# Performance work log

Hardware: AMD Instinct MI355X
Metric: run time of the kernel (lower is better)

## Reference

```python
import jax, jax.numpy as jnp
import numpy as np

B, D, S, NSYM, V, T = 4096, 128, 16, 128, 128, 8
EPS = 1e-6; ACT_TH = 0.9999; GBS = 0.8; CC = 0.01
sg = jax.lax.stop_gradient


def clin(xr, xi, Wr, Wi):
    # ComplexLinear: torch Linear applies x @ W.T
    return xr @ Wr.T - xi @ Wi.T, xi @ Wr.T + xr @ Wi.T


def cnorm(zr, zi, scale, shift):
    # ComplexLayerNorm: normalize magnitude (torch .var is unbiased -> ddof=1), keep phase
    mag = jnp.sqrt(zr * zr + zi * zi) + EPS
    mean = mag.mean(-1, keepdims=True)
    var = jnp.var(mag, axis=-1, ddof=1, keepdims=True)
    nm = (mag - mean) / jnp.sqrt(var + EPS) * scale + shift
    ph = jnp.arctan2(zi, zr)
    return nm * jnp.cos(ph), nm * jnp.sin(ph)


def modrelu(zr, zi, bias):
    norm = jnp.sqrt(zr * zr + zi * zi) + EPS
    s = jax.nn.relu(norm + bias) / norm
    return zr * s, zi * s


def setup_inputs():
    key = jax.random.key(0)
    ks = jax.random.split(key, 18)
    n = lambda k, sh, s=0.05: jax.random.normal(k, sh, jnp.float32) * s
    return dict(
        input_ids=jax.random.randint(ks[0], (B, 1), 0, V),
        emb_mag=n(ks[1], (V, D), 1.0),
        emb_phase=n(ks[2], (V, D), 1.0),
        cell_Wr=n(ks[3], (D, D), 0.08), cell_Wi=n(ks[4], (D, D), 0.08),
        ln_scale=jnp.ones((D,), jnp.float32), ln_shift=jnp.zeros((D,), jnp.float32),
        mod_bias=jnp.zeros((D,), jnp.float32),
        Wh=n(ks[5], (1, 2 * D)), bh=jnp.full((1,), -2.0, jnp.float32),
        Ws=n(ks[6], (3, 2 * D)), bs=jnp.zeros((3,), jnp.float32),
        Wq_r=n(ks[7], (D, D), 0.08), Wq_i=n(ks[8], (D, D), 0.08),
        Wk_r=n(ks[9], (D, D), 0.08), Wk_i=n(ks[10], (D, D), 0.08),
        Wv_r=n(ks[11], (D, D), 0.08), Wv_i=n(ks[12], (D, D), 0.08),
        codebook=jax.random.uniform(ks[13], (NSYM, 2 * D), jnp.float32, -0.5, 0.5),
        adjacency=n(ks[14], (NSYM, NSYM), 0.1),
        Wd=n(ks[15], (V, 2 * D)), bd=jnp.zeros((V,), jnp.float32),
    )


def _forward(input_ids, emb_mag, emb_phase, cell_Wr, cell_Wi, ln_scale, ln_shift,
             mod_bias, Wh, bh, Ws, bs, Wq_r, Wq_i, Wk_r, Wk_i, Wv_r, Wv_i,
             codebook, adjacency, Wd, bd):
    idx = input_ids[:, 0]                              # (B,)
    r = emb_mag[idx]; th = emb_phase[idx]
    zr, zi = r * jnp.cos(th), r * jnp.sin(th)          # complex embed (B,D)
    bsz = zr.shape[0]
    stack_mem = jnp.zeros((bsz, S, 2 * D), jnp.float32)
    ptr = jnp.zeros((bsz, S), jnp.float32).at[:, 0].set(1.0)
    halting = jnp.zeros((bsz, 1), jnp.float32)
    remain = jnp.ones((bsz, 1), jnp.float32)
    zwr = jnp.zeros_like(zr); zwi = jnp.zeros_like(zi)
    vq_total = jnp.zeros((bsz,), jnp.float32)
    eth_total = jnp.zeros((bsz,), jnp.float32)
    ponder = jnp.zeros((bsz, 1), jnp.float32)
    cur_sym = None
    scale = D ** -0.5
    for t in range(T):  # fixed small recursion depth, unrolled
        # AdaptiveRecursiveCell
        pr, pi = clin(zr, zi, cell_Wr, cell_Wi)
        pr, pi = cnorm(pr, pi, ln_scale, ln_shift)
        pr, pi = modrelu(pr, pi, mod_bias)
        qr, qi = clin(pr, pi, Wq_r, Wq_i)
        kr, ki = clin(pr, pi, Wk_r, Wk_i)
        vr, vi = clin(pr, pi, Wv_r, Wv_i)
        qf = jnp.concatenate([qr, qi], -1)
        kf = jnp.concatenate([kr, ki], -1)
        attn = jax.nn.softmax(qf @ kf.T * scale, axis=-1)  # (B,B) cross-batch attn, as in source
        ar, ai2 = attn @ vr, attn @ vi
        zf = jnp.concatenate([ar, ai2], -1)                # (B,2D)
        p_halt = jax.nn.sigmoid(zf @ Wh.T + bh)            # (B,1)
        ctrl = jax.nn.softmax(zf @ Ws.T + bs, axis=-1)     # (B,3)
        # DifferentiableStack soft push/pop
        push, pop, noop = ctrl[:, 0:1], ctrl[:, 1:2], ctrl[:, 2:3]
        ptr_up = jnp.roll(ptr, 1, axis=1)
        ptr_dn = jnp.roll(ptr, -1, axis=1)
        new_ptr = push * ptr_up + pop * ptr_dn + noop * ptr
        new_ptr = new_ptr / (new_ptr.sum(1, keepdims=True) + EPS)
        wm = (push * ptr_up)[:, :, None]                   # (B,S,1) soft write mask
        stack_mem = wm * zf[:, None, :] + stack_mem * (1.0 - wm)
        read = (stack_mem * new_ptr[:, :, None]).sum(1)    # (B,2D)
        ptr = new_ptr
        cr, ci = ar + read[:, :D], ai2 + read[:, D:]
        # GraphMemoryVQ
        cf = jnp.concatenate([cr, ci], -1)
        d = (cf * cf).sum(-1, keepdims=True) + (codebook * codebook).sum(-1) - 2.0 * cf @ codebook.T
        if cur_sym is not None:
            d = d - GBS * jax.nn.sigmoid(adjacency[cur_sym])
        sym = jnp.argmin(d, axis=-1)
        zq = codebook[sym]
        vq_loss = ((zq - sg(cf)) ** 2).mean(-1) + CC * ((sg(zq) - cf) ** 2).mean(-1)
        zq_st = cf + sg(zq - cf)                            # straight-through
        # EthicalConstraint: CE(adjacency[prev], curr)
        if cur_sym is None:
            eth = jnp.zeros((bsz,), jnp.float32)
        else:
            logp = jax.nn.log_softmax(adjacency[cur_sym], axis=-1)
            eth = -jnp.take_along_axis(logp, sym[:, None], axis=-1)[:, 0]
        eth_total = eth_total + eth
        cur_sym = sym
        zr = 0.7 * cr + 0.3 * zq_st[:, :D]
        zi = 0.7 * ci + 0.3 * zq_st[:, D:]
        # ACT halting (standard ACT weighting; final step takes remainder)
        still = (halting < ACT_TH).astype(jnp.float32)
        p = p_halt * still
        if t == T - 1:
            p = remain
        halting = halting + p
        remain = remain - p
        zwr = zwr + p * zr
        zwi = zwi + p * zi
        vq_total = vq_total + vq_loss
        ponder = ponder + still
    logits = jnp.concatenate([zwr, zwi], -1) @ Wd.T + bd    # (B, V)
    return logits, vq_total, eth_total, ponder[:, 0]


def reference(input_ids, emb_mag, emb_phase, cell_Wr, cell_Wi, ln_scale, ln_shift,
              mod_bias, Wh, bh, Ws, bs, Wq_r, Wq_i, Wk_r, Wk_i, Wv_r, Wv_i,
              codebook, adjacency, Wd, bd):
    return _forward(input_ids, emb_mag, emb_phase, cell_Wr, cell_Wi, ln_scale, ln_shift,
                    mod_bias, Wh, bh, Ws, bs, Wq_r, Wq_i, Wk_r, Wk_i, Wv_r, Wv_i,
                    codebook, adjacency, Wd, bd)
```

## Files before the change

kernel.cpp:

```cpp
#include <hip/hip_runtime.h>
#include <hip/hip_bf16.h>
#include <math.h>

#define B 4096
#define D 128
#define TWO_D 256
#define S_SLOTS 16
#define NSYM 128
#define V_OUT 128
#define T_STEPS 8
#define EPS 1e-6f
#define ACT_TH 0.9999f
#define GBS 0.8f
#define CC 0.01f
#define SCALE 0.08838834764831845f

#define NCHUNK 8
#define CHUNK (B / NCHUNK)
#define QT 32
#define KT 64

typedef short s16x8 __attribute__((ext_vector_type(8)));
typedef float f32x4 __attribute__((ext_vector_type(4)));
#define MFMA16(A, Bb, C) __builtin_amdgcn_mfma_f32_16x16x32_bf16(A, Bb, C, 0, 0, 0)

__device__ __forceinline__ unsigned short f2bf(float x) {
  __bf16 h = (__bf16)x;
  return *(unsigned short*)&h;
}
__device__ __forceinline__ float bf2f(unsigned short u) {
  __bf16 h = *(__bf16*)&u;
  return (float)h;
}

__device__ __forceinline__ float combine_w(const float* __restrict__ Wr,
                                           const float* __restrict__ Wi,
                                           int j, int k) {
  if (j < D) return (k < D) ? Wr[j * D + k] : -Wi[j * D + (k - D)];
  return (k < D) ? Wi[(j - D) * D + k] : Wr[(j - D) * D + (k - D)];
}

__global__ __launch_bounds__(256) void build_weights(
    const float* __restrict__ cell_Wr, const float* __restrict__ cell_Wi,
    const float* __restrict__ Wq_r, const float* __restrict__ Wq_i,
    const float* __restrict__ Wk_r, const float* __restrict__ Wk_i,
    const float* __restrict__ Wv_r, const float* __restrict__ Wv_i,
    const float* __restrict__ codebook,
    unsigned short* __restrict__ cellWH, unsigned short* __restrict__ cellWL,
    unsigned short* __restrict__ qkvWH, unsigned short* __restrict__ qkvWL,
    float* __restrict__ cbsq) {
  int e = blockIdx.x * 256 + threadIdx.x;
  int j = e >> 8, k = e & 255;
  float v = combine_w(cell_Wr, cell_Wi, j, k);
  unsigned short hh = f2bf(v);
  cellWH[e] = hh; cellWL[e] = f2bf(v - bf2f(hh));
  v = combine_w(Wq_r, Wq_i, j, k);
  hh = f2bf(v); qkvWH[e] = hh; qkvWL[e] = f2bf(v - bf2f(hh));
  v = combine_w(Wk_r, Wk_i, j, k);
  hh = f2bf(v); qkvWH[65536 + e] = hh; qkvWL[65536 + e] = f2bf(v - bf2f(hh));
  v = combine_w(Wv_r, Wv_i, j, k);
  hh = f2bf(v); qkvWH[131072 + e] = hh; qkvWL[131072 + e] = f2bf(v - bf2f(hh));
  if (blockIdx.x == 0 && threadIdx.x < NSYM) {
    float s = 0.f;
    for (int c = 0; c < TWO_D; c++) {
      float cv = codebook[threadIdx.x * TWO_D + c];
      s += cv * cv;
    }
    cbsq[threadIdx.x] = s;
  }
}

__global__ __launch_bounds__(128) void init_state(
    const int* __restrict__ input_ids, const float* __restrict__ emb_mag,
    const float* __restrict__ emb_phase,
    unsigned short* __restrict__ zfH, unsigned short* __restrict__ zfL,
    float* __restrict__ ptrb, float* __restrict__ halting,
    float* __restrict__ remain, float* __restrict__ vq,
    float* __restrict__ eth, float* __restrict__ ponder,
    float* __restrict__ zw, float* __restrict__ stack) {
  int b = blockIdx.x, tid = threadIdx.x;
  int idx = input_ids[b];
  float rr = emb_mag[idx * D + tid];
  float th = emb_phase[idx * D + tid];
  float zr = rr * cosf(th), zi = rr * sinf(th);
  unsigned short hh = f2bf(zr);
  zfH[(size_t)b * TWO_D + tid] = hh;
  zfL[(size_t)b * TWO_D + tid] = f2bf(zr - bf2f(hh));
  hh = f2bf(zi);
  zfH[(size_t)b * TWO_D + D + tid] = hh;
  zfL[(size_t)b * TWO_D + D + tid] = f2bf(zi - bf2f(hh));
  zw[(size_t)b * TWO_D + tid] = 0.f;
  zw[(size_t)b * TWO_D + D + tid] = 0.f;
  if (tid < S_SLOTS) ptrb[b * S_SLOTS + tid] = (tid == 0) ? 1.f : 0.f;
  if (tid == 0) {
    halting[b] = 0.f; remain[b] = 1.f;
    vq[b] = 0.f; eth[b] = 0.f; ponder[b] = 0.f;
  }
  for (int k = tid; k < S_SLOTS * TWO_D; k += 128)
    stack[(size_t)b * S_SLOTS * TWO_D + k] = 0.f;
}

template <int MODE>
__global__ __launch_bounds__(256) void gemm_mfma(
    const unsigned short* __restrict__ AH, const unsigned short* __restrict__ AL,
    const unsigned short* __restrict__ WH, const unsigned short* __restrict__ WL,
    float* __restrict__ Cf,
    unsigned short* __restrict__ qH_, unsigned short* __restrict__ qL_,
    unsigned short* __restrict__ kH_, unsigned short* __restrict__ kL_,
    unsigned short* __restrict__ vtH_, unsigned short* __restrict__ vtL_) {
  const int tid = threadIdx.x;
  const int w = tid >> 6, lane = tid & 63, r = lane & 15, h = lane >> 4;
  const int m0 = blockIdx.x * 32 + (w & 1) * 16;
  const int n0g = blockIdx.y * 64 + (w >> 1) * 32;
  f32x4 acc[2];
  acc[0] = f32x4{0.f, 0.f, 0.f, 0.f};
  acc[1] = f32x4{0.f, 0.f, 0.f, 0.f};
  const size_t abase = (size_t)(m0 + r) * TWO_D;
  const size_t wb0 = (size_t)(n0g + r) * TWO_D;
  const size_t wb1 = (size_t)(n0g + 16 + r) * TWO_D;
#pragma unroll
  for (int kf = 0; kf < 8; kf++) {
    s16x8 ah = *(const s16x8*)&AH[abase + kf * 32 + h * 8];
    s16x8 al = *(const s16x8*)&AL[abase + kf * 32 + h * 8];
    s16x8 b0h = *(const s16x8*)&WH[wb0 + kf * 32 + h * 8];
    s16x8 b0l = *(const s16x8*)&WL[wb0 + kf * 32 + h * 8];
    s16x8 b1h = *(const s16x8*)&WH[wb1 + kf * 32 + h * 8];
    s16x8 b1l = *(const s16x8*)&WL[wb1 + kf * 32 + h * 8];
    acc[0] = MFMA16(ah, b0h, acc[0]);
    acc[0] = MFMA16(ah, b0l, acc[0]);
    acc[0] = MFMA16(al, b0h, acc[0]);
    acc[1] = MFMA16(ah, b1h, acc[1]);
    acc[1] = MFMA16(ah, b1l, acc[1]);
    acc[1] = MFMA16(al, b1h, acc[1]);
  }
#pragma unroll
  for (int ct = 0; ct < 2; ct++) {
    int col = n0g + ct * 16 + r;
#pragma unroll
    for (int reg = 0; reg < 4; reg++) {
      int row = m0 + h * 4 + reg;
      float val = acc[ct][reg];
      if (MODE == 0) {
        Cf[(size_t)row * TWO_D + col] = val;
      } else {
        int buf = col >> 8;
        int c = col & 255;
        if (buf == 0) {
          float v2 = val * SCALE;
          unsigned short hh = f2bf(v2);
          qH_[(size_t)row * TWO_D + c] = hh;
          qL_[(size_t)row * TWO_D + c] = f2bf(v2 - bf2f(hh));
        } else if (buf == 1) {
          unsigned short hh = f2bf(val);
          kH_[(size_t)row * TWO_D + c] = hh;
          kL_[(size_t)row * TWO_D + c] = f2bf(val - bf2f(hh));
        } else {
          unsigned short hh = f2bf(val);
          vtH_[(size_t)c * B + row] = hh;
          vtL_[(size_t)c * B + row] = f2bf(val - bf2f(hh));
        }
      }
    }
  }
}

__global__ __launch_bounds__(128) void cnorm_modrelu(
    const float* __restrict__ pf, const float* __restrict__ ln_scale,
    const float* __restrict__ ln_shift, const float* __restrict__ mod_bias,
    unsigned short* __restrict__ pfH, unsigned short* __restrict__ pfL) {
  int b = blockIdx.x, d = threadIdx.x;
  __shared__ float red[128];
  float pr = pf[(size_t)b * TWO_D + d];
  float pi = pf[(size_t)b * TWO_D + D + d];
  float h = sqrtf(pr * pr + pi * pi);
  float mag = h + EPS;
  red[d] = mag;
  __syncthreads();
  for (int s = 64; s > 0; s >>= 1) {
    if (d < s) red[d] += red[d + s];
    __syncthreads();
  }
  float mean = red[0] * (1.f / 128.f);
  __syncthreads();
  float dm = mag - mean;
  red[d] = dm * dm;
  __syncthreads();
  for (int s = 64; s > 0; s >>= 1) {
    if (d < s) red[d] += red[d + s];
    __syncthreads();
  }
  float var = red[0] * (1.f / 127.f);
  float nm = dm * (1.f / sqrtf(var + EPS)) * ln_scale[d] + ln_shift[d];
  float cph, sph;
  if (h > 0.f) { cph = pr / h; sph = pi / h; } else { cph = 1.f; sph = 0.f; }
  float zr = nm * cph, zi = nm * sph;
  float norm = sqrtf(zr * zr + zi * zi) + EPS;
  float s = fmaxf(norm + mod_bias[d], 0.f) / norm;
  float or_ = zr * s, oi_ = zi * s;
  unsigned short hh = f2bf(or_);
  pfH[(size_t)b * TWO_D + d] = hh;
  pfL[(size_t)b * TWO_D + d] = f2bf(or_ - bf2f(hh));
  hh = f2bf(oi_);
  pfH[(size_t)b * TWO_D + D + d] = hh;
  pfL[(size_t)b * TWO_D + D + d] = f2bf(oi_ - bf2f(hh));
}

__global__ __launch_bounds__(256) void flash_mfma(
    const unsigned short* __restrict__ qH, const unsigned short* __restrict__ qL,
    const unsigned short* __restrict__ kH, const unsigned short* __restrict__ kL,
    const unsigned short* __restrict__ vtH, const unsigned short* __restrict__ vtL,
    float* __restrict__ Opart, float* __restrict__ mpart,
    float* __restrict__ lpart) {
  __shared__ float m_lds[QT], corr_lds[QT];
  __shared__ float wmax[QT][2], lpart_lds[QT][2];
  __shared__ unsigned short Ph[QT][72], Pl[QT][72];
  const int tid = threadIdx.x;
  const int w = tid >> 6, lane = tid & 63;
  const int r = lane & 15, h = lane >> 4;
  const int qt = w & 1, kh = w >> 1;
  const int bid = blockIdx.x;
  const int chunk = bid & 7;
  const int q0 = (bid >> 3) * QT;

  s16x8 qfh[8], qfl[8];
  {
    const size_t base = (size_t)(q0 + qt * 16 + r) * TWO_D;
#pragma unroll
    for (int kf = 0; kf < 8; kf++) {
      qfh[kf] = *(const s16x8*)&qH[base + kf * 32 + h * 8];
      qfl[kf] = *(const s16x8*)&qL[base + kf * 32 + h * 8];
    }
  }
  f32x4 o[2][4];
#pragma unroll
  for (int qi = 0; qi < 2; qi++)
#pragma unroll
    for (int dt = 0; dt < 4; dt++) o[qi][dt] = f32x4{0.f, 0.f, 0.f, 0.f};
  float l_loc[4] = {0.f, 0.f, 0.f, 0.f};
  if (tid < QT) m_lds[tid] = -1e30f;
  __syncthreads();

  for (int kt = 0; kt < CHUNK / KT; kt++) {
    const int j0 = chunk * CHUNK + kt * KT;
    f32x4 sacc[2];
    sacc[0] = f32x4{0.f, 0.f, 0.f, 0.f};
    sacc[1] = f32x4{0.f, 0.f, 0.f, 0.f};
    const size_t kb0 = (size_t)(j0 + kh * 32 + r) * TWO_D;
    const size_t kb1 = (size_t)(j0 + kh * 32 + 16 + r) * TWO_D;
#pragma unroll
    for (int kf = 0; kf < 8; kf++) {
      s16x8 b0h = *(const s16x8*)&kH[kb0 + kf * 32 + h * 8];
      s16x8 b0l = *(const s16x8*)&kL[kb0 + kf * 32 + h * 8];
      s16x8 b1h = *(const s16x8*)&kH[kb1 + kf * 32 + h * 8];
      s16x8 b1l = *(const s16x8*)&kL[kb1 + kf * 32 + h * 8];
      sacc[0] = MFMA16(qfh[kf], b0h, sacc[0]);
      sacc[0] = MFMA16(qfh[kf], b0l, sacc[0]);
      sacc[0] = MFMA16(qfl[kf], b0h, sacc[0]);
      sacc[1] = MFMA16(qfh[kf], b1h, sacc[1]);
      sacc[1] = MFMA16(qfh[kf], b1l, sacc[1]);
      sacc[1] = MFMA16(qfl[kf], b1h, sacc[1]);
    }
#pragma unroll
    for (int reg = 0; reg < 4; reg++) {
      float v = fmaxf(sacc[0][reg], sacc[1][reg]);
      v = fmaxf(v, __shfl_xor(v, 1));
      v = fmaxf(v, __shfl_xor(v, 2));
      v = fmaxf(v, __shfl_xor(v, 4));
      v = fmaxf(v, __shfl_xor(v, 8));
      if (r == 0) wmax[qt * 16 + h * 4 + reg][kh] = v;
    }
    __syncthreads();
    if (lane < 8) {
      int row = w * 8 + lane;
      float mo = m_lds[row];
      float mn = fmaxf(mo, fmaxf(wmax[row][0], wmax[row][1]));
      corr_lds[row] = __expf(mo - mn);
      m_lds[row] = mn;
    }
    __syncthreads();
#pragma unroll
    for (int reg = 0; reg < 4; reg++) {
      int row = qt * 16 + h * 4 + reg;
      float mrow = m_lds[row];
      float p0 = __expf(sacc[0][reg] - mrow);
      float p1 = __expf(sacc[1][reg] - mrow);
      float rs = p0 + p1;
      rs += __shfl_xor(rs, 1);
      rs += __shfl_xor(rs, 2);
      rs += __shfl_xor(rs, 4);
      rs += __shfl_xor(rs, 8);
      l_loc[reg] = l_loc[reg] * corr_lds[row] + rs;
      unsigned short p0h = f2bf(p0), p1h = f2bf(p1);
      Ph[row][kh * 32 + r] = p0h;
      Pl[row][kh * 32 + r] = f2bf(p0 - bf2f(p0h));
      Ph[row][kh * 32 + 16 + r] = p1h;
      Pl[row][kh * 32 + 16 + r] = f2bf(p1 - bf2f(p1h));
    }
#pragma unroll
    for (int qi = 0; qi < 2; qi++)
#pragma unroll
      for (int reg = 0; reg < 4; reg++) {
        float c = corr_lds[qi * 16 + h * 4 + reg];
#pragma unroll
        for (int dt = 0; dt < 4; dt++) o[qi][dt][reg] *= c;
      }
    __syncthreads();
#pragma unroll
    for (int kf2 = 0; kf2 < 2; kf2++) {
      s16x8 pa_h[2], pa_l[2];
#pragma unroll
      for (int qi = 0; qi < 2; qi++) {
        pa_h[qi] = *(const s16x8*)&Ph[qi * 16 + r][kf2 * 32 + h * 8];
        pa_l[qi] = *(const s16x8*)&Pl[qi * 16 + r][kf2 * 32 + h * 8];
      }
#pragma unroll
      for (int dt = 0; dt < 4; dt++) {
        const size_t vb = (size_t)(w * 64 + dt * 16 + r) * B + j0 + kf2 * 32 + h * 8;
        s16x8 vh = *(const s16x8*)&vtH[vb];
        s16x8 vl = *(const s16x8*)&vtL[vb];
#pragma unroll
        for (int qi = 0; qi < 2; qi++) {
          o[qi][dt] = MFMA16(pa_h[qi], vh, o[qi][dt]);
          o[qi][dt] = MFMA16(pa_h[qi], vl, o[qi][dt]);
          o[qi][dt] = MFMA16(pa_l[qi], vh, o[qi][dt]);
        }
      }
    }
  }
  if (r == 0) {
#pragma unroll
    for (int reg = 0; reg < 4; reg++)
      lpart_lds[qt * 16 + h * 4 + reg][kh] = l_loc[reg];
  }
  __syncthreads();
  const size_t obase = (size_t)chunk * B + q0;
#pragma unroll
  for (int qi = 0; qi < 2; qi++)
#pragma unroll
    for (int reg = 0; reg < 4; reg++) {
      float* dst = &Opart[(obase + qi * 16 + h * 4 + reg) * TWO_D + w * 64 + r];
#pragma unroll
      for (int dt = 0; dt < 4; dt++) dst[dt * 16] = o[qi][dt][reg];
    }
  if (w == 0 && lane < QT) {
    mpart[chunk * B + q0 + lane] = m_lds[lane];
    lpart[chunk * B + q0 + lane] = lpart_lds[lane][0] + lpart_lds[lane][1];
  }
}

__global__ __launch_bounds__(256) void merge_attn(
    const float* __restrict__ Opart, const float* __restrict__ mpart,
    const float* __restrict__ lpart, float* __restrict__ af) {
  int b = blockIdx.x, c = threadIdx.x;
  float M = -1e30f;
#pragma unroll
  for (int ch = 0; ch < NCHUNK; ch++) M = fmaxf(M, mpart[ch * B + b]);
  float l = 0.f, o = 0.f;
#pragma unroll
  for (int ch = 0; ch < NCHUNK; ch++) {
    float wgt = __expf(mpart[ch * B + b] - M);
    l += lpart[ch * B + b] * wgt;
    o += Opart[((size_t)ch * B + b) * TWO_D + c] * wgt;
  }
  af[(size_t)b * TWO_D + c] = o / l;
}

__global__ __launch_bounds__(256) void step_kernel(
    const float* __restrict__ af, unsigned short* __restrict__ zfH,
    unsigned short* __restrict__ zfL, float* __restrict__ stack,
    float* __restrict__ ptrb, float* __restrict__ halting,
    float* __restrict__ remain, float* __restrict__ vq,
    float* __restrict__ eth, float* __restrict__ ponder,
    float* __restrict__ zw, int* __restrict__ cursym,
    const float* __restrict__ Wh, const float* __restrict__ bh,
    const float* __restrict__ Ws3, const float* __restrict__ bs3,
    const float* __restrict__ codebook, const float* __restrict__ cbsq,
    const float* __restrict__ adjacency, int t) {
  const int b = blockIdx.x, tid = threadIdx.x;
  __shared__ float cf_sh[TWO_D];
  __shared__ float r0[256], r1[256], r2[256], r3[256];
  __shared__ float nptr_sh[S_SLOTS], wm_sh[S_SLOTS];
  __shared__ float dist_sh[NSYM];
  __shared__ int idx_sh[NSYM];
  __shared__ float sc_sh[8];

  const float z_c = af[(size_t)b * TWO_D + tid];
  const int cs_old = (t > 0) ? cursym[b] : 0;

  r0[tid] = z_c * Wh[tid];
  r1[tid] = z_c * Ws3[tid];
  r2[tid] = z_c * Ws3[TWO_D + tid];
  r3[tid] = z_c * Ws3[2 * TWO_D + tid];
  __syncthreads();
  for (int s = 128; s > 0; s >>= 1) {
    if (tid < s) {
      r0[tid] += r0[tid + s]; r1[tid] += r1[tid + s];
      r2[tid] += r2[tid + s]; r3[tid] += r3[tid + s];
    }
    __syncthreads();
  }
  if (tid == 0) {
    float ph = 1.f / (1.f + expf(-(r0[0] + bh[0])));
    float l0 = r1[0] + bs3[0], l1 = r2[0] + bs3[1], l2 = r3[0] + bs3[2];
    float mx = fmaxf(l0, fmaxf(l1, l2));
    float e0 = expf(l0 - mx), e1 = expf(l1 - mx), e2 = expf(l2 - mx);
    float inv = 1.f / (e0 + e1 + e2);
    sc_sh[0] = e0 * inv; sc_sh[1] = e1 * inv; sc_sh[2] = e2 * inv;
    sc_sh[3] = ph;
  }
  __syncthreads();
  float push = sc_sh[0], pop = sc_sh[1], noop = sc_sh[2], p_halt = sc_sh[3];
  if (tid < S_SLOTS) {
    float pc = ptrb[b * S_SLOTS + tid];
    float pu = ptrb[b * S_SLOTS + ((tid + 15) & 15)];
    float pd = ptrb[b * S_SLOTS + ((tid + 1) & 15)];
    float raw = push * pu + pop * pd + noop * pc;
    float wmv = push * pu;
    float ssum = raw;
    for (int off = 1; off < 16; off <<= 1) ssum += __shfl_xor(ssum, off);
    float np_ = raw / (ssum + EPS);
    nptr_sh[tid] = np_;
    wm_sh[tid] = wmv;
    ptrb[b * S_SLOTS + tid] = np_;
  }
  __syncthreads();
  float acc = 0.f;
#pragma unroll
  for (int s = 0; s < S_SLOTS; s++) {
    size_t ix = ((size_t)(b * S_SLOTS + s)) * TWO_D + tid;
    float v = stack[ix];
    float wv = wm_sh[s];
    v = wv * z_c + v * (1.f - wv);
    stack[ix] = v;
    acc += v * nptr_sh[s];
  }
  float cf_c = z_c + acc;
  cf_sh[tid] = cf_c;
  r0[tid] = cf_c * cf_c;
  __syncthreads();
  for (int s = 128; s > 0; s >>= 1) {
    if (tid < s) r0[tid] += r0[tid + s];
    __syncthreads();
  }
  float cfsq = r0[0];
  if (tid < NSYM) {
    const float* cb = codebook + (size_t)tid * TWO_D;
    float dot = 0.f;
#pragma unroll 8
    for (int c = 0; c < TWO_D; c++) dot += cf_sh[c] * cb[c];
    float dval = cfsq + cbsq[tid] - 2.f * dot;
    if (t > 0) {
      float a = adjacency[cs_old * NSYM + tid];
      dval -= GBS * (1.f / (1.f + expf(-a)));
    }
    dist_sh[tid] = dval;
    idx_sh[tid] = tid;
  }
  __syncthreads();
  for (int s = 64; s > 0; s >>= 1) {
    if (tid < s) {
      float dA = dist_sh[tid], dB = dist_sh[tid + s];
      int iA = idx_sh[tid], iB = idx_sh[tid + s];
      if (dB < dA || (dB == dA && iB < iA)) {
        dist_sh[tid] = dB; idx_sh[tid] = iB;
      }
    }
    __syncthreads();
  }
  const int sym = idx_sh[0];
  const float zq_c = codebook[(size_t)sym * TWO_D + tid];
  float diff = zq_c - cf_c;
  r1[tid] = diff * diff;
  r2[tid] = (t > 0 && tid < NSYM) ? adjacency[cs_old * NSYM + tid] : -1e30f;
  __syncthreads();
  for (int s = 128; s > 0; s >>= 1) {
    if (tid < s) {
      r1[tid] += r1[tid + s];
      r2[tid] = fmaxf(r2[tid], r2[tid + s]);
    }
    __syncthreads();
  }
  float amax = r2[0];
  r3[tid] = (t > 0 && tid < NSYM) ? expf(adjacency[cs_old * NSYM + tid] - amax)
                                  : 0.f;
  __syncthreads();
  for (int s = 128; s > 0; s >>= 1) {
    if (tid < s) r3[tid] += r3[tid + s];
    __syncthreads();
  }
  if (tid == 0) {
    float vql = (1.f + CC) * (r1[0] * (1.f / (float)TWO_D));
    float h = halting[b], rem = remain[b];
    float still = (h < ACT_TH) ? 1.f : 0.f;
    float p = (t == T_STEPS - 1) ? rem : p_halt * still;
    halting[b] = h + p;
    remain[b] = rem - p;
    ponder[b] += still;
    vq[b] += vql;
    if (t > 0) {
      float asym = adjacency[cs_old * NSYM + sym];
      eth[b] += (amax + logf(r3[0]) - asym);
    }
    cursym[b] = sym;
    sc_sh[4] = p;
  }
  __syncthreads();
  float p = sc_sh[4];
  float znew = 0.7f * cf_c + 0.3f * zq_c;
  unsigned short hh = f2bf(znew);
  zfH[(size_t)b * TWO_D + tid] = hh;
  zfL[(size_t)b * TWO_D + tid] = f2bf(znew - bf2f(hh));
  zw[(size_t)b * TWO_D + tid] += p * znew;
}

__global__ __launch_bounds__(128) void logits_kernel(
    const float* __restrict__ zw, const float* __restrict__ Wd,
    const float* __restrict__ bd, const float* __restrict__ vq,
    const float* __restrict__ eth, const float* __restrict__ ponder,
    float* __restrict__ out) {
  int b = blockIdx.x, tid = threadIdx.x;
  __shared__ float zsh[TWO_D];
  zsh[tid] = zw[(size_t)b * TWO_D + tid];
  zsh[tid + D] = zw[(size_t)b * TWO_D + D + tid];
  __syncthreads();
  const float* wrow = Wd + (size_t)tid * TWO_D;
  float dot = 0.f;
#pragma unroll 8
  for (int c = 0; c < TWO_D; c++) dot += zsh[c] * wrow[c];
  out[(size_t)b * V_OUT + tid] = dot + bd[tid];
  if (tid == 0) {
    out[(size_t)B * V_OUT + b] = vq[b];
    out[(size_t)B * V_OUT + B + b] = eth[b];
    out[(size_t)B * V_OUT + 2 * B + b] = ponder[b];
  }
}

extern "C" void kernel_launch(void* const* d_in, const int* in_sizes, int n_in,
                              void* d_out, int out_size, void* d_ws,
                              size_t ws_size, hipStream_t stream) {
  const int* input_ids = (const int*)d_in[0];
  const float* emb_mag = (const float*)d_in[1];
  const float* emb_phase = (const float*)d_in[2];
  const float* cell_Wr = (const float*)d_in[3];
  const float* cell_Wi = (const float*)d_in[4];
  const float* ln_scale = (const float*)d_in[5];
  const float* ln_shift = (const float*)d_in[6];
  const float* mod_bias = (const float*)d_in[7];
  const float* Wh = (const float*)d_in[8];
  const float* bh = (const float*)d_in[9];
  const float* Ws3 = (const float*)d_in[10];
  const float* bs3 = (const float*)d_in[11];
  const float* Wq_r = (const float*)d_in[12];
  const float* Wq_i = (const float*)d_in[13];
  const float* Wk_r = (const float*)d_in[14];
  const float* Wk_i = (const float*)d_in[15];
  const float* Wv_r = (const float*)d_in[16];
  const float* Wv_i = (const float*)d_in[17];
  const float* codebook = (const float*)d_in[18];
  const float* adjacency = (const float*)d_in[19];
  const float* Wd = (const float*)d_in[20];
  const float* bd = (const float*)d_in[21];
  float* out = (float*)d_out;

  char* w = (char*)d_ws;
  size_t off = 0;
  auto alloc = [&](size_t bytes) {
    char* p = w + off;
    off += (bytes + 255) & ~(size_t)255;
    return p;
  };
  unsigned short* cellWH = (unsigned short*)alloc(65536 * 2);
  unsigned short* cellWL = (unsigned short*)alloc(65536 * 2);
  unsigned short* qkvWH = (unsigned short*)alloc(3 * 65536 * 2);
  unsigned short* qkvWL = (unsigned short*)alloc(3 * 65536 * 2);
  float* cbsq = (float*)alloc(NSYM * 4);
  unsigned short* zfH = (unsigned short*)alloc((size_t)B * TWO_D * 2);
  unsigned short* zfL = (unsigned short*)alloc((size_t)B * TWO_D * 2);
  float* pf = (float*)alloc((size_t)B * TWO_D * 4);
  unsigned short* pfH = (unsigned short*)alloc((size_t)B * TWO_D * 2);
  unsigned short* pfL = (unsigned short*)alloc((size_t)B * TWO_D * 2);
  unsigned short* qHb = (unsigned short*)alloc((size_t)B * TWO_D * 2);
  unsigned short* qLb = (unsigned short*)alloc((size_t)B * TWO_D * 2);
  unsigned short* kHb = (unsigned short*)alloc((size_t)B * TWO_D * 2);
  unsigned short* kLb = (unsigned short*)alloc((size_t)B * TWO_D * 2);
  unsigned short* vtH = (unsigned short*)alloc((size_t)B * TWO_D * 2);
  unsigned short* vtL = (unsigned short*)alloc((size_t)B * TWO_D * 2);
  float* af = (float*)alloc((size_t)B * TWO_D * 4);
  float* zw_ = (float*)alloc((size_t)B * TWO_D * 4);
  float* Opart = (float*)alloc((size_t)NCHUNK * B * TWO_D * 4);
  float* mpart = (float*)alloc((size_t)NCHUNK * B * 4);
  float* lpart = (float*)alloc((size_t)NCHUNK * B * 4);
  float* ptrb = (float*)alloc((size_t)B * S_SLOTS * 4);
  float* halting = (float*)alloc(B * 4);
  float* remain = (float*)alloc(B * 4);
  float* vqb = (float*)alloc(B * 4);
  float* ethb = (float*)alloc(B * 4);
  float* ponderb = (float*)alloc(B * 4);
  int* cursym = (int*)alloc(B * 4);
  float* stack = (float*)alloc((size_t)B * S_SLOTS * TWO_D * 4);

  build_weights<<<256, 256, 0, stream>>>(cell_Wr, cell_Wi, Wq_r, Wq_i, Wk_r,
                                         Wk_i, Wv_r, Wv_i, codebook, cellWH,
                                         cellWL, qkvWH, qkvWL, cbsq);
  init_state<<<B, 128, 0, stream>>>(input_ids, emb_mag, emb_phase, zfH, zfL,
                                    ptrb, halting, remain, vqb, ethb, ponderb,
                                    zw_, stack);
  for (int t = 0; t < T_STEPS; t++) {
    gemm_mfma<0><<<dim3(B / 32, 4), 256, 0, stream>>>(
        zfH, zfL, cellWH, cellWL, pf, nullptr, nullptr, nullptr, nullptr,
        nullptr, nullptr);
    cnorm_modrelu<<<B, 128, 0, stream>>>(pf, ln_scale, ln_shift, mod_bias, pfH,
                                         pfL);
    gemm_mfma<1><<<dim3(B / 32, 12), 256, 0, stream>>>(
        pfH, pfL, qkvWH, qkvWL, nullptr, qHb, qLb, kHb, kLb, vtH, vtL);
    flash_mfma<<<dim3((B / QT) * NCHUNK), 256, 0, stream>>>(
        qHb, qLb, kHb, kLb, vtH, vtL, Opart, mpart, lpart);
    merge_attn<<<B, 256, 0, stream>>>(Opart, mpart, lpart, af);
    step_kernel<<<B, 256, 0, stream>>>(af, zfH, zfL, stack, ptrb, halting,
                                       remain, vqb, ethb, ponderb, zw_, cursym,
                                       Wh, bh, Ws3, bs3, codebook, cbsq,
                                       adjacency, t);
  }
  logits_kernel<<<B, 128, 0, stream>>>(zw_, Wd, bd, vqb, ethb, ponderb, out);
}
```

Before: 3.008 ms.

## Restructure flash attention so each wave owns 16 query rows without block syncs

Replaces the block-cooperative flash attention, where four waves shared the max and sum reductions through LDS and three __syncthreads per key tile, with a wave-independent design. Each wave handles 16 query rows over all 256 output columns, keeps the running max and sum in registers, and passes P through a private LDS slice. The change targets barrier and LDS-reduction overhead. In exchange each wave loads every K and V tile itself, so the block no longer shares those loads across waves, and the output accumulator grows to 16 tiles per wave, raising register pressure.

```diff
diff --git a/kernel.cpp b/kernel.cpp
--- a/kernel.cpp
+++ b/kernel.cpp
@@ -17,8 +17,6 @@
 
 #define NCHUNK 8
 #define CHUNK (B / NCHUNK)
-#define QT 32
-#define KT 64
 
 typedef short s16x8 __attribute__((ext_vector_type(8)));
 typedef float f32x4 __attribute__((ext_vector_type(4)));
@@ -205,146 +203,106 @@
   pfL[(size_t)b * TWO_D + D + d] = f2bf(oi_ - bf2f(hh));
 }
 
-__global__ __launch_bounds__(256) void flash_mfma(
+__global__ __launch_bounds__(256) void flash_wave(
     const unsigned short* __restrict__ qH, const unsigned short* __restrict__ qL,
     const unsigned short* __restrict__ kH, const unsigned short* __restrict__ kL,
     const unsigned short* __restrict__ vtH, const unsigned short* __restrict__ vtL,
     float* __restrict__ Opart, float* __restrict__ mpart,
     float* __restrict__ lpart) {
-  __shared__ float m_lds[QT], corr_lds[QT];
-  __shared__ float wmax[QT][2], lpart_lds[QT][2];
-  __shared__ unsigned short Ph[QT][72], Pl[QT][72];
+  __shared__ unsigned short PwH[4][16][40];
+  __shared__ unsigned short PwL[4][16][40];
   const int tid = threadIdx.x;
   const int w = tid >> 6, lane = tid & 63;
   const int r = lane & 15, h = lane >> 4;
-  const int qt = w & 1, kh = w >> 1;
   const int bid = blockIdx.x;
   const int chunk = bid & 7;
-  const int q0 = (bid >> 3) * QT;
+  const int q0 = (bid >> 3) * 64 + w * 16;
 
   s16x8 qfh[8], qfl[8];
   {
-    const size_t base = (size_t)(q0 + qt * 16 + r) * TWO_D;
+    const size_t base = (size_t)(q0 + r) * TWO_D;
 #pragma unroll
     for (int kf = 0; kf < 8; kf++) {
       qfh[kf] = *(const s16x8*)&qH[base + kf * 32 + h * 8];
       qfl[kf] = *(const s16x8*)&qL[base + kf * 32 + h * 8];
     }
   }
-  f32x4 o[2][4];
-#pragma unroll
-  for (int qi = 0; qi < 2; qi++)
-#pragma unroll
-    for (int dt = 0; dt < 4; dt++) o[qi][dt] = f32x4{0.f, 0.f, 0.f, 0.f};
-  float l_loc[4] = {0.f, 0.f, 0.f, 0.f};
-  if (tid < QT) m_lds[tid] = -1e30f;
-  __syncthreads();
-
-  for (int kt = 0; kt < CHUNK / KT; kt++) {
-    const int j0 = chunk * CHUNK + kt * KT;
-    f32x4 sacc[2];
-    sacc[0] = f32x4{0.f, 0.f, 0.f, 0.f};
-    sacc[1] = f32x4{0.f, 0.f, 0.f, 0.f};
-    const size_t kb0 = (size_t)(j0 + kh * 32 + r) * TWO_D;
-    const size_t kb1 = (size_t)(j0 + kh * 32 + 16 + r) * TWO_D;
+  f32x4 o[16];
+#pragma unroll
+  for (int dt = 0; dt < 16; dt++) o[dt] = f32x4{0.f, 0.f, 0.f, 0.f};
+  float m_i[4] = {-1e30f, -1e30f, -1e30f, -1e30f};
+  float l_i[4] = {0.f, 0.f, 0.f, 0.f};
+
+  for (int kt = 0; kt < CHUNK / 32; kt++) {
+    const int j0 = chunk * CHUNK + kt * 32;
+    f32x4 s0 = f32x4{0.f, 0.f, 0.f, 0.f};
+    f32x4 s1 = f32x4{0.f, 0.f, 0.f, 0.f};
+    const size_t kb0 = (size_t)(j0 + r) * TWO_D;
+    const size_t kb1 = (size_t)(j0 + 16 + r) * TWO_D;
 #pragma unroll
     for (int kf = 0; kf < 8; kf++) {
       s16x8 b0h = *(const s16x8*)&kH[kb0 + kf * 32 + h * 8];
       s16x8 b0l = *(const s16x8*)&kL[kb0 + kf * 32 + h * 8];
       s16x8 b1h = *(const s16x8*)&kH[kb1 + kf * 32 + h * 8];
       s16x8 b1l = *(const s16x8*)&kL[kb1 + kf * 32 + h * 8];
-      sacc[0] = MFMA16(qfh[kf], b0h, sacc[0]);
-      sacc[0] = MFMA16(qfh[kf], b0l, sacc[0]);
-      sacc[0] = MFMA16(qfl[kf], b0h, sacc[0]);
-      sacc[1] = MFMA16(qfh[kf], b1h, sacc[1]);
-      sacc[1] = MFMA16(qfh[kf], b1l, sacc[1]);
-      sacc[1] = MFMA16(qfl[kf], b1h, sacc[1]);
+      s0 = MFMA16(qfh[kf], b0h, s0);
+      s0 = MFMA16(qfh[kf], b0l, s0);
+      s0 = MFMA16(qfl[kf], b0h, s0);
+      s1 = MFMA16(qfh[kf], b1h, s1);
+      s1 = MFMA16(qfh[kf], b1l, s1);
+      s1 = MFMA16(qfl[kf], b1h, s1);
     }
 #pragma unroll
     for (int reg = 0; reg < 4; reg++) {
-      float v = fmaxf(sacc[0][reg], sacc[1][reg]);
-      v = fmaxf(v, __shfl_xor(v, 1));
-      v = fmaxf(v, __shfl_xor(v, 2));
-      v = fmaxf(v, __shfl_xor(v, 4));
-      v = fmaxf(v, __shfl_xor(v, 8));
-      if (r == 0) wmax[qt * 16 + h * 4 + reg][kh] = v;
-    }
-    __syncthreads();
-    if (lane < 8) {
-      int row = w * 8 + lane;
-      float mo = m_lds[row];
-      float mn = fmaxf(mo, fmaxf(wmax[row][0], wmax[row][1]));
-      corr_lds[row] = __expf(mo - mn);
-      m_lds[row] = mn;
-    }
-    __syncthreads();
-#pragma unroll
-    for (int reg = 0; reg < 4; reg++) {
-      int row = qt * 16 + h * 4 + reg;
-      float mrow = m_lds[row];
-      float p0 = __expf(sacc[0][reg] - mrow);
-      float p1 = __expf(sacc[1][reg] - mrow);
+      float mm = fmaxf(s0[reg], s1[reg]);
+      mm = fmaxf(mm, __shfl_xor(mm, 1));
+      mm = fmaxf(mm, __shfl_xor(mm, 2));
+      mm = fmaxf(mm, __shfl_xor(mm, 4));
+      mm = fmaxf(mm, __shfl_xor(mm, 8));
+      float mnew = fmaxf(m_i[reg], mm);
+      float corr = __expf(m_i[reg] - mnew);
+      float p0 = __expf(s0[reg] - mnew);
+      float p1 = __expf(s1[reg] - mnew);
       float rs = p0 + p1;
       rs += __shfl_xor(rs, 1);
       rs += __shfl_xor(rs, 2);
       rs += __shfl_xor(rs, 4);
       rs += __shfl_xor(rs, 8);
-      l_loc[reg] = l_loc[reg] * corr_lds[row] + rs;
-      unsigned short p0h = f2bf(p0), p1h = f2bf(p1);
-      Ph[row][kh * 32 + r] = p0h;
-      Pl[row][kh * 32 + r] = f2bf(p0 - bf2f(p0h));
-      Ph[row][kh * 32 + 16 + r] = p1h;
-      Pl[row][kh * 32 + 16 + r] = f2bf(p1 - bf2f(p1h));
-    }
-#pragma unroll
-    for (int qi = 0; qi < 2; qi++)
-#pragma unroll
-      for (int reg = 0; reg < 4; reg++) {
-        float c = corr_lds[qi * 16 + h * 4 + reg];
-#pragma unroll
-        for (int dt = 0; dt < 4; dt++) o[qi][dt][reg] *= c;
-      }
-    __syncthreads();
-#pragma unroll
-    for (int kf2 = 0; kf2 < 2; kf2++) {
-      s16x8 pa_h[2], pa_l[2];
-#pragma unroll
-      for (int qi = 0; qi < 2; qi++) {
-        pa_h[qi] = *(const s16x8*)&Ph[qi * 16 + r][kf2 * 32 + h * 8];
-        pa_l[qi] = *(const s16x8*)&Pl[qi * 16 + r][kf2 * 32 + h * 8];
-      }
-#pragma unroll
-      for (int dt = 0; dt < 4; dt++) {
-        const size_t vb = (size_t)(w * 64 + dt * 16 + r) * B + j0 + kf2 * 32 + h * 8;
-        s16x8 vh = *(const s16x8*)&vtH[vb];
-        s16x8 vl = *(const s16x8*)&vtL[vb];
-#pragma unroll
-        for (int qi = 0; qi < 2; qi++) {
-          o[qi][dt] = MFMA16(pa_h[qi], vh, o[qi][dt]);
-          o[qi][dt] = MFMA16(pa_h[qi], vl, o[qi][dt]);
-          o[qi][dt] = MFMA16(pa_l[qi], vh, o[qi][dt]);
-        }
-      }
-    }
-  }
-  if (r == 0) {
-#pragma unroll
-    for (int reg = 0; reg < 4; reg++)
-      lpart_lds[qt * 16 + h * 4 + reg][kh] = l_loc[reg];
-  }
-  __syncthreads();
+      l_i[reg] = l_i[reg] * corr + rs;
+      m_i[reg] = mnew;
+      const int row = h * 4 + reg;
+      unsigned short ph = f2bf(p0);
+      PwH[w][row][r] = ph;
+      PwL[w][row][r] = f2bf(p0 - bf2f(ph));
+      ph = f2bf(p1);
+      PwH[w][row][16 + r] = ph;
+      PwL[w][row][16 + r] = f2bf(p1 - bf2f(ph));
+#pragma unroll
+      for (int dt = 0; dt < 16; dt++) o[dt][reg] *= corr;
+    }
+    s16x8 pah = *(const s16x8*)&PwH[w][r][h * 8];
+    s16x8 pal = *(const s16x8*)&PwL[w][r][h * 8];
+#pragma unroll
+    for (int dt = 0; dt < 16; dt++) {
+      const size_t vb = (size_t)(dt * 16 + r) * B + j0 + h * 8;
+      s16x8 vh = *(const s16x8*)&vtH[vb];
+      s16x8 vl = *(const s16x8*)&vtL[vb];
+      o[dt] = MFMA16(pah, vh, o[dt]);
+      o[dt] = MFMA16(pah, vl, o[dt]);
+      o[dt] = MFMA16(pal, vh, o[dt]);
+    }
+  }
   const size_t obase = (size_t)chunk * B + q0;
 #pragma unroll
-  for (int qi = 0; qi < 2; qi++)
-#pragma unroll
-    for (int reg = 0; reg < 4; reg++) {
-      float* dst = &Opart[(obase + qi * 16 + h * 4 + reg) * TWO_D + w * 64 + r];
-#pragma unroll
-      for (int dt = 0; dt < 4; dt++) dst[dt * 16] = o[qi][dt][reg];
-    }
-  if (w == 0 && lane < QT) {
-    mpart[chunk * B + q0 + lane] = m_lds[lane];
-    lpart[chunk * B + q0 + lane] = lpart_lds[lane][0] + lpart_lds[lane][1];
+  for (int reg = 0; reg < 4; reg++) {
+    const int row = h * 4 + reg;
+    float* dst = &Opart[(obase + row) * TWO_D + r];
+#pragma unroll
+    for (int dt = 0; dt < 16; dt++) dst[dt * 16] = o[dt][reg];
+    if (r == 0) {
+      mpart[chunk * B + q0 + row] = m_i[reg];
+      lpart[chunk * B + q0 + row] = l_i[reg];
+    }
   }
 }
 
@@ -613,7 +571,7 @@
                                          pfL);
     gemm_mfma<1><<<dim3(B / 32, 12), 256, 0, stream>>>(
         pfH, pfL, qkvWH, qkvWL, nullptr, qHb, qLb, kHb, kLb, vtH, vtL);
-    flash_mfma<<<dim3((B / QT) * NCHUNK), 256, 0, stream>>>(
+    flash_wave<<<dim3((B / 64) * NCHUNK), 256, 0, stream>>>(
         qHb, qLb, kHb, kLb, vtH, vtL, Opart, mpart, lpart);
     merge_attn<<<B, 256, 0, stream>>>(Opart, mpart, lpart, af);
     step_kernel<<<B, 256, 0, stream>>>(af, zfH, zfL, stack, ptrb, halting,
```

New measurement: 3.714 ms. 1.23x slower.
